# Performance work log

Measured on AMD Instinct MI355X. Metric: run time of the kernel, lower is better.

The kernel has to match this reference:

```python
import jax, jax.numpy as jnp
import numpy as np
from jax import lax

B, S, T = 16, 128, 64
V, E, H = 32000, 256, 256

def setup_inputs() -> dict:
    key = jax.random.key(0)
    ks = jax.random.split(key, 22)
    w = lambda k, shape: jax.random.normal(k, shape, dtype=jnp.float32) * 0.05
    return {
        "input_seq": jax.random.randint(ks[0], (B, S), 0, V),
        "target_seq": jax.random.randint(ks[1], (B, T), 0, V),
        "enc_emb": w(ks[2], (V, E)),
        "enc_Wih": w(ks[3], (4 * H, E)),
        "enc_Whh": w(ks[4], (4 * H, H)),
        "enc_b": w(ks[5], (4 * H,)),
        "dec_emb": w(ks[6], (V, E)),
        "Wq": w(ks[7], (H, H)), "bq": w(ks[8], (H,)),
        "Wk": w(ks[9], (H, H)), "bk": w(ks[10], (H,)),
        "Wv": w(ks[11], (H, H)), "bv": w(ks[12], (H,)),
        "Wo": w(ks[13], (H, H)), "bo": w(ks[14], (H,)),
        "dec_Wih": w(ks[15], (4 * H, E + H)),
        "dec_Whh": w(ks[16], (4 * H, H)),
        "dec_b": w(ks[17], (4 * H,)),
        "Wout": w(ks[18], (V, H)), "bout": w(ks[19], (V,)),
    }

def _lstm_step(Wih, Whh, b, x, h, c):
    # PyTorch LSTM gate order: i, f, g, o
    g = x @ Wih.T + h @ Whh.T + b
    i, f, gg, o = jnp.split(g, 4, axis=-1)
    c = jax.nn.sigmoid(f) * c + jax.nn.sigmoid(i) * jnp.tanh(gg)
    h = jax.nn.sigmoid(o) * jnp.tanh(c)
    return h, c

def reference(input_seq, target_seq, enc_emb, enc_Wih, enc_Whh, enc_b,
              dec_emb, Wq, bq, Wk, bk, Wv, bv, Wo, bo,
              dec_Wih, dec_Whh, dec_b, Wout, bout):
    Bn = input_seq.shape[0]
    # ---- encoder LSTM over source ----
    src = enc_emb[input_seq]                      # [B,S,E]
    h0 = jnp.zeros((Bn, H), src.dtype)
    c0 = jnp.zeros((Bn, H), src.dtype)

    def enc_step(carry, x_t):
        h, c = carry
        h, c = _lstm_step(enc_Wih, enc_Whh, enc_b, x_t, h, c)
        return (h, c), h
    (h_enc, c_enc), enc_hs = lax.scan(enc_step, (h0, c0), src.transpose(1, 0, 2))
    enc_out = enc_hs.transpose(1, 0, 2)           # [B,S,H]

    # ---- precompute attention K/V projections (enc_out is fixed) ----
    K = enc_out @ Wk.T + bk                       # [B,S,H]
    Vp = enc_out @ Wv.T + bv                      # [B,S,H]
    scale = 1.0 / jnp.sqrt(jnp.asarray(H, src.dtype))

    # ---- teacher-forced decode loop (sequential via scan) ----
    tok = dec_emb[target_seq[:, :-1]]             # [B,T-1,E]

    def dec_step(carry, x_t):
        h, c = carry
        q = h @ Wq.T + bq                         # [B,H]  query = current hidden
        scores = jnp.einsum('bh,bsh->bs', q, K) * scale
        attn = jax.nn.softmax(scores, axis=-1)
        ctx = jnp.einsum('bs,bsh->bh', attn, Vp)
        ctx = ctx @ Wo.T + bo                     # MHA out-projection
        h, c = _lstm_step(dec_Wih, dec_Whh, dec_b,
                          jnp.concatenate([x_t, ctx], axis=-1), h, c)
        logits = h @ Wout.T + bout                # [B,V]
        return (h, c), logits

    _, logits = lax.scan(dec_step, (h_enc, c_enc), tok.transpose(1, 0, 2))
    return logits.transpose(1, 0, 2)              # [B,T-1,V]
```

## Files before the change

### kernel.cpp

```cpp
#include <hip/hip_runtime.h>

typedef short bh8 __attribute__((ext_vector_type(8)));
typedef float f32x4 __attribute__((ext_vector_type(4)));

#define DEVI __device__ __forceinline__

union U8 { bh8 v; unsigned short u[8]; };

DEVI float bf2f(unsigned short u){
  unsigned int x = ((unsigned int)u) << 16;
  return __builtin_bit_cast(float, x);
}
DEVI unsigned short f2bf(float f){
  unsigned int u = __builtin_bit_cast(unsigned int, f);
  u += 0x7fffu + ((u >> 16) & 1u);
  return (unsigned short)(u >> 16);
}
DEVI float sigm(float x){ return 1.0f/(1.0f + __expf(-x)); }

DEVI f32x4 MFMA(bh8 a, bh8 b, f32x4 c){
  return __builtin_amdgcn_mfma_f32_16x16x32_bf16(a, b, c, 0, 0, 0);
}

DEVI unsigned int ld_sc0(const unsigned int* p){
  unsigned int v;
  asm volatile("global_load_dword %0, %1, off sc0\n\ts_waitcnt vmcnt(0)"
               : "=v"(v) : "v"(p) : "memory");
  return v;
}
DEVI void st_plain(unsigned int* p, unsigned int v){
  asm volatile("global_store_dword %0, %1, off" :: "v"(p), "v"(v) : "memory");
}

DEVI float poll2(const unsigned int* fastp, const unsigned int* slowp){
  unsigned int v;
  for (int it = 0; it < (1 << 23); ++it){
    v = ld_sc0(fastp);
    if (v != 0xFFFFFFFFu) return __builtin_bit_cast(float, v);
    v = __hip_atomic_load(slowp, __ATOMIC_RELAXED, __HIP_MEMORY_SCOPE_AGENT);
    if (v != 0xFFFFFFFFu) return __builtin_bit_cast(float, v);
  }
  return __builtin_bit_cast(float, v);
}

DEVI void conv_dev(const float* src, unsigned short* dst, int rows, int rstride,
                   int lblk, int nblk){
  int tid = threadIdx.x;
  size_t n = (size_t)rows * 128;
  for (size_t i = (size_t)lblk * 256 + tid; i < n; i += (size_t)nblk * 256){
    size_t r = i >> 7; int c = ((int)(i & 127)) * 2;
    const float* s = src + r * (size_t)rstride + c;
    unsigned int hp = (unsigned int)f2bf(s[0]) | ((unsigned int)f2bf(s[1]) << 16);
    *(unsigned int*)(dst + r * 256 + c) = hp;
  }
}

DEVI void fold_dev(const float* A, int offA, int sAm, int sAk,
                   const float* Bm, int offB, int sBn, int sBk,
                   const float* addM, float* Cf, unsigned short* Cb,
                   int M, int N, int lblk, int nblk){
  int tid = threadIdx.x;
  for (int i = lblk * 256 + tid; i < M * N; i += nblk * 256){
    int m = i / N, n = i - m * N;
    const float* a = A + offA + (size_t)m * sAm;
    const float* b = Bm + offB + (size_t)n * sBn;
    float acc = 0.f;
    for (int k = 0; k < 256; ++k) acc += a[(size_t)k * sAk] * b[(size_t)k * sBk];
    if (addM) acc += addM[m];
    if (Cf) Cf[i] = acc;
    if (Cb) Cb[i] = f2bf(acc);
  }
}

__global__ __launch_bounds__(256) void k_prepA(const int* input_seq, const int* target_seq,
      const float* enc_emb, const float* dec_emb,
      const float* enc_Wih, const float* dec_Wih, const float* Wout,
      const float* enc_Whh, const float* dec_Whh,
      const float* Wq, const float* Wk, const float* bq, const float* bk,
      const float* Wo, const float* bo, const float* dec_b,
      unsigned short* src_bf, unsigned short* tok_bf,
      unsigned short* wih_bf, unsigned short* wxd_bf, unsigned short* wout_bf,
      unsigned short* whhE_bf, unsigned short* whhD_bf,
      float* Gf, unsigned short* A3bf, float* c3f, float* c4f, float* c5f, float* xdb){
  int blk = blockIdx.x, tid = threadIdx.x;
  if (blk < 512){
    for (int r = 0; r < 4; ++r){
      int m = blk * 4 + r;
      int idx = input_seq[m];
      src_bf[(size_t)m * 256 + tid] = f2bf(enc_emb[(size_t)idx * 256 + tid]);
    }
  } else if (blk < 768){
    int lb = blk - 512;
    for (int r = 0; r < 4; ++r){
      int m = lb * 4 + r;
      if (m < 1008){
        int bb = m / 63, t = m - bb * 63;
        int idx = target_seq[bb * 64 + t];
        tok_bf[(size_t)m * 256 + tid] = f2bf(dec_emb[(size_t)idx * 256 + tid]);
      } else tok_bf[(size_t)m * 256 + tid] = 0;
    }
  }
  else if (blk < 896)  conv_dev(enc_Wih, wih_bf, 1024, 256, blk - 768, 128);
  else if (blk < 1024) conv_dev(dec_Wih, wxd_bf, 1024, 512, blk - 896, 128);
  else if (blk < 2048) conv_dev(Wout,    wout_bf, 32000, 256, blk - 1024, 1024);
  else if (blk < 2176) conv_dev(enc_Whh, whhE_bf, 1024, 256, blk - 2048, 128);
  else if (blk < 2304) conv_dev(dec_Whh, whhD_bf, 1024, 256, blk - 2176, 128);
  else if (blk < 3328) fold_dev(dec_Wih,256,512,1, Wo,0,1,256, nullptr, Gf,nullptr, 1024,256, blk - 2304, 1024);
  else if (blk < 3584) fold_dev(Wq,0,1,256,        Wk,0,1,256, nullptr, nullptr,A3bf, 256,256, blk - 3328, 256);
  else if (blk == 3584) fold_dev(bk,0,0,1, Wq,0,1,256, nullptr, c3f,nullptr, 1,256, 0, 1);
  else if (blk == 3585) fold_dev(bq,0,0,1, Wk,0,1,256, nullptr, c4f,nullptr, 1,256, 0, 1);
  else if (blk == 3586) fold_dev(bq,0,0,1, bk,0,0,1,   nullptr, c5f,nullptr, 1,1,   0, 1);
  else                  fold_dev(dec_Wih,256,512,1, bo,0,0,1, dec_b, xdb,nullptr, 1024,1, blk - 3587, 4);
}

__global__ __launch_bounds__(256) void k_prepB(const float* Gf, const float* Wv,
      const float* bv, unsigned short* A2bf, float* xdb){
  int blk = blockIdx.x;
  if (blk < 512) fold_dev(Gf,0,256,1, Wv,0,1,256, nullptr, nullptr,A2bf, 1024,256, blk, 512);
  else           fold_dev(Gf,0,256,1, bv,0,0,1,   xdb,     xdb,nullptr, 1024,1,   blk - 512, 4);
}

DEVI void gemm_tile(const unsigned short* __restrict__ A,
      const unsigned short* __restrict__ Bw, const float* __restrict__ bias,
      float* __restrict__ Cf, unsigned short* __restrict__ Cb, int Mlog, int N,
      int tmi, int tni, unsigned short* lA, unsigned short* lB){
  int tid = threadIdx.x;
  int lane = tid & 63, wave = tid >> 6;
  int wm = wave >> 1, wn = wave & 1;
  int kg = lane >> 4, l15 = lane & 15;
  size_t tm = tmi, tn = tni;
  f32x4 acc[4][4];
#pragma unroll
  for (int i = 0; i < 4; ++i)
#pragma unroll
    for (int j = 0; j < 4; ++j) acc[i][j] = (f32x4){0.f, 0.f, 0.f, 0.f};

  for (int ks = 0; ks < 8; ++ks){
    __syncthreads();
#pragma unroll
    for (int i = 0; i < 2; ++i){
      int slot = i * 256 + tid;
      int r = slot >> 2, sg = slot & 3;
      bh8 va = *reinterpret_cast<const bh8*>(A + (tm * 128 + r) * 256 + ks * 32 + sg * 8);
      *reinterpret_cast<bh8*>((char*)lA + r * 64 + ((sg ^ (r & 3)) << 4)) = va;
      bh8 vb = *reinterpret_cast<const bh8*>(Bw + (tn * 128 + r) * 256 + ks * 32 + sg * 8);
      *reinterpret_cast<bh8*>((char*)lB + r * 64 + ((sg ^ (r & 3)) << 4)) = vb;
    }
    __syncthreads();
    bh8 af[4], bfr[4];
#pragma unroll
    for (int mi = 0; mi < 4; ++mi){
      int r = wm * 64 + mi * 16 + l15;
      af[mi] = *reinterpret_cast<const bh8*>((char*)lA + r * 64 + ((kg ^ (r & 3)) << 4));
    }
#pragma unroll
    for (int ni = 0; ni < 4; ++ni){
      int r = wn * 64 + ni * 16 + l15;
      bfr[ni] = *reinterpret_cast<const bh8*>((char*)lB + r * 64 + ((kg ^ (r & 3)) << 4));
    }
#pragma unroll
    for (int mi = 0; mi < 4; ++mi)
#pragma unroll
      for (int ni = 0; ni < 4; ++ni)
        acc[mi][ni] = MFMA(af[mi], bfr[ni], acc[mi][ni]);
  }
#pragma unroll
  for (int ni = 0; ni < 4; ++ni){
    int col = (int)tn * 128 + wn * 64 + ni * 16 + l15;
    float bv = bias ? bias[col] : 0.f;
#pragma unroll
    for (int mi = 0; mi < 4; ++mi){
#pragma unroll
      for (int rg = 0; rg < 4; ++rg){
        int row = (int)tm * 128 + wm * 64 + mi * 16 + kg * 4 + rg;
        if (row < Mlog){
          float v = acc[mi][ni][rg] + bv;
          if (Cb) Cb[(size_t)row * N + col] = f2bf(v);
          else    Cf[(size_t)row * N + col] = v;
        }
      }
    }
  }
}

__global__ __launch_bounds__(256) void k_gemm(const unsigned short* __restrict__ A,
      const unsigned short* __restrict__ Bw, const float* __restrict__ bias,
      float* __restrict__ Cf, unsigned short* __restrict__ Cb, int Mlog, int N){
  __shared__ __align__(16) unsigned short lA[128 * 32];
  __shared__ __align__(16) unsigned short lB[128 * 32];
  gemm_tile(A, Bw, bias, Cf, Cb, Mlog, N, blockIdx.y, blockIdx.x, lA, lB);
}

__global__ __launch_bounds__(256) void k_gemmAB(const unsigned short* src_bf,
      const unsigned short* wih_bf, const float* enc_b, float* Xg,
      const unsigned short* tok_bf, const unsigned short* wxd_bf, const float* xdb, float* Xd){
  __shared__ __align__(16) unsigned short lA[128 * 32];
  __shared__ __align__(16) unsigned short lB[128 * 32];
  int blk = blockIdx.x;
  if (blk < 128) gemm_tile(src_bf, wih_bf, enc_b, Xg, nullptr, 2048, 1024, blk >> 3, blk & 7, lA, lB);
  else { int l = blk - 128; gemm_tile(tok_bf, wxd_bf, xdb, Xd, nullptr, 1024, 1024, l >> 3, l & 7, lA, lB); }
}

__global__ __launch_bounds__(256) void k_gemmPost(const unsigned short* enc_bf,
      const unsigned short* A3bf, const float* c3f, unsigned short* KWb,
      const unsigned short* A2bf, unsigned short* VWWT,
      const float* c4f, const float* c5f, float* sbf){
  __shared__ __align__(16) unsigned short lA[128 * 32];
  __shared__ __align__(16) unsigned short lB[128 * 32];
  int blk = blockIdx.x, tid = threadIdx.x;
  if (blk < 32) gemm_tile(enc_bf, A3bf, c3f, nullptr, KWb, 2048, 256, blk >> 1, blk & 1, lA, lB);
  else if (blk < 160){ int l = blk - 32; gemm_tile(A2bf, enc_bf, nullptr, nullptr, VWWT, 1024, 2048, l >> 4, l & 15, lA, lB); }
  else {
    int m = (blk - 160) * 256 + tid;
    const unsigned short* e = enc_bf + (size_t)m * 256;
    float a = 0.f;
    for (int k = 0; k < 256; ++k) a += bf2f(e[k]) * c4f[k];
    sbf[m] = a + c5f[0];
  }
}

__global__ __launch_bounds__(256) void k_enc_g(const unsigned short* __restrict__ Whh_bf,
      const float* __restrict__ Xg, unsigned short* __restrict__ enc_bf,
      float* hbEf, float* hbEs, float* hbDf, float* hbDs, float* cfin){
  __shared__ __align__(16) unsigned short Ws[128 * 256];
  __shared__ __align__(16) float h_l[256];
  __shared__ float part[256];
  int tid = threadIdx.x, blk = blockIdx.x;
  int b = blk & 15, sub = blk >> 4, j0 = sub * 32;
  int lr = tid >> 1, kh = tid & 1;

  for (int i = 0; i < 16; ++i){
    int id = i * 256 + tid;
    int slr = id >> 5, c = id & 31;
    int R = (slr >> 5) * 256 + j0 + (slr & 31);
    bh8 v = *reinterpret_cast<const bh8*>(Whh_bf + (size_t)R * 256 + c * 8);
    *reinterpret_cast<bh8*>((char*)Ws + slr * 512 + ((c ^ (slr & 31)) << 4)) = v;
  }
  h_l[tid] = 0.f;
  float creg = 0.f;
  int Rr = (lr >> 5) * 256 + j0 + (lr & 31);
  __syncthreads();

  for (int t = 0; t < 128; ++t){
    float xg = (kh == 0) ? Xg[(size_t)(b * 128 + t) * 1024 + Rr] : 0.f;
    if (t > 0 && (tid >> 5) != sub)
      h_l[tid] = poll2((const unsigned int*)hbEf + (size_t)t * 4096 + b * 256 + tid,
                       (const unsigned int*)hbEs + (size_t)t * 4096 + b * 256 + tid);
    __syncthreads();
    {
      float acc = xg;
#pragma unroll
      for (int ci = 0; ci < 16; ++ci){
        int chunk = kh * 16 + ci;
        U8 w; w.v = *reinterpret_cast<const bh8*>((char*)Ws + lr * 512 + ((chunk ^ (lr & 31)) << 4));
        float4 ha = *(const float4*)(h_l + chunk * 8);
        float4 hb = *(const float4*)(h_l + chunk * 8 + 4);
        acc += ha.x*bf2f(w.u[0]) + ha.y*bf2f(w.u[1]) + ha.z*bf2f(w.u[2]) + ha.w*bf2f(w.u[3]);
        acc += hb.x*bf2f(w.u[4]) + hb.y*bf2f(w.u[5]) + hb.z*bf2f(w.u[6]) + hb.w*bf2f(w.u[7]);
      }
      part[tid] = acc;
    }
    __syncthreads();
    if (tid < 32){
      float gi = part[tid*2]      + part[tid*2 + 1];
      float gf = part[(32+tid)*2] + part[(32+tid)*2 + 1];
      float gg = part[(64+tid)*2] + part[(64+tid)*2 + 1];
      float go = part[(96+tid)*2] + part[(96+tid)*2 + 1];
      float c = sigm(gf) * creg + sigm(gi) * tanhf(gg);
      float h = sigm(go) * tanhf(c);
      creg = c;
      int j = j0 + tid;
      h_l[j] = h;
      unsigned int hb = __builtin_bit_cast(unsigned int, h);
      if (t < 127){
        st_plain((unsigned int*)hbEf + (size_t)(t + 1) * 4096 + b * 256 + j, hb);
        __hip_atomic_store((unsigned int*)hbEs + (size_t)(t + 1) * 4096 + b * 256 + j, hb,
                           __ATOMIC_RELAXED, __HIP_MEMORY_SCOPE_AGENT);
      } else {
        hbDf[b * 256 + j] = h;
        hbDs[b * 256 + j] = h;
        cfin[b * 256 + j] = c;
      }
      enc_bf[(size_t)(b * 128 + t) * 256 + j] = f2bf(h);
    }
  }
}

__global__ __launch_bounds__(256) void k_dec_g(const unsigned short* __restrict__ Whh_bf,
      const float* __restrict__ Xd, const unsigned short* __restrict__ KW,
      const unsigned short* __restrict__ VWWT, const float* __restrict__ sb,
      float* hbDf, float* hbDs, const float* __restrict__ cfin,
      unsigned short* __restrict__ Hs){
  __shared__ __align__(16) unsigned short KW_l[128 * 256];
  __shared__ __align__(16) unsigned short Ws[128 * 256];
  __shared__ __align__(16) float h_l[256];
  __shared__ float part[256];
  __shared__ float sc_l[128];
  __shared__ float at_l[128];
  __shared__ float red0, red1;
  int tid = threadIdx.x, blk = blockIdx.x;
  int b = blk & 15, sub = blk >> 4, j0 = sub * 32;
  int ss = tid >> 1, kh = tid & 1;
  int lr = ss;

  for (int i = 0; i < 16; ++i){
    int id = i * 256 + tid;
    int row = id >> 5, c = id & 31;
    bh8 v = *reinterpret_cast<const bh8*>(KW + (size_t)(b * 128 + row) * 256 + c * 8);
    *reinterpret_cast<bh8*>((char*)KW_l + row * 512 + ((c ^ (row & 31)) << 4)) = v;
  }
  for (int i = 0; i < 16; ++i){
    int id = i * 256 + tid;
    int row = id >> 5, c = id & 31;
    int R = (row >> 5) * 256 + j0 + (row & 31);
    bh8 v = *reinterpret_cast<const bh8*>(Whh_bf + (size_t)R * 256 + c * 8);
    *reinterpret_cast<bh8*>((char*)Ws + row * 512 + ((c ^ (row & 31)) << 4)) = v;
  }
  int Rr = (lr >> 5) * 256 + j0 + (lr & 31);
  U8 vw[8];
#pragma unroll
  for (int ci = 0; ci < 8; ++ci)
    vw[ci].v = *reinterpret_cast<const bh8*>(VWWT + (size_t)Rr * 2048 + b * 128 + kh * 64 + ci * 8);
  float sbreg = (tid < 128) ? sb[b * 128 + tid] : 0.f;
  float creg = (tid < 32) ? cfin[b * 256 + j0 + tid] : 0.f;
  __syncthreads();

  for (int t = 0; t < 63; ++t){
    float xdreg = (kh == 0) ? Xd[(size_t)(b * 63 + t) * 1024 + Rr] : 0.f;
    if (t == 0 || (tid >> 5) != sub)
      h_l[tid] = poll2((const unsigned int*)hbDf + (size_t)t * 4096 + b * 256 + tid,
                       (const unsigned int*)hbDs + (size_t)t * 4096 + b * 256 + tid);
    __syncthreads();
    {
      float a = 0.f;
#pragma unroll
      for (int i = 0; i < 16; ++i){
        int ch = kh * 16 + i;
        U8 ku; ku.v = *reinterpret_cast<const bh8*>((char*)KW_l + ss * 512 + ((ch ^ (ss & 31)) << 4));
        const float* hp = h_l + ch * 8;
#pragma unroll
        for (int q = 0; q < 8; ++q) a += hp[q] * bf2f(ku.u[q]);
      }
      part[tid] = a;
    }
    __syncthreads();
    if (tid < 128) sc_l[tid] = (part[2 * tid] + part[2 * tid + 1] + sbreg) * 0.0625f;
    __syncthreads();
    if (tid < 64){
      float m = fmaxf(sc_l[tid], sc_l[tid + 64]);
      for (int o = 32; o; o >>= 1) m = fmaxf(m, __shfl_xor(m, o));
      if (tid == 0) red0 = m;
    }
    __syncthreads();
    if (tid < 128) sc_l[tid] = __expf(sc_l[tid] - red0);
    __syncthreads();
    if (tid < 64){
      float s = sc_l[tid] + sc_l[tid + 64];
      for (int o = 32; o; o >>= 1) s += __shfl_xor(s, o);
      if (tid == 0) red1 = s;
    }
    __syncthreads();
    if (tid < 128) at_l[tid] = sc_l[tid] / red1;
    __syncthreads();
    {
      float acc = xdreg;
#pragma unroll
      for (int ci = 0; ci < 16; ++ci){
        int ch = kh * 16 + ci;
        U8 w; w.v = *reinterpret_cast<const bh8*>((char*)Ws + lr * 512 + ((ch ^ (lr & 31)) << 4));
        float4 ha = *(const float4*)(h_l + ch * 8);
        float4 hb = *(const float4*)(h_l + ch * 8 + 4);
        acc += ha.x*bf2f(w.u[0]) + ha.y*bf2f(w.u[1]) + ha.z*bf2f(w.u[2]) + ha.w*bf2f(w.u[3]);
        acc += hb.x*bf2f(w.u[4]) + hb.y*bf2f(w.u[5]) + hb.z*bf2f(w.u[6]) + hb.w*bf2f(w.u[7]);
      }
#pragma unroll
      for (int ci = 0; ci < 8; ++ci){
        const float* ap = at_l + kh * 64 + ci * 8;
#pragma unroll
        for (int q = 0; q < 8; ++q) acc += ap[q] * bf2f(vw[ci].u[q]);
      }
      part[tid] = acc;
    }
    __syncthreads();
    if (tid < 32){
      float gi = part[tid*2]      + part[tid*2 + 1];
      float gf = part[(32+tid)*2] + part[(32+tid)*2 + 1];
      float gg = part[(64+tid)*2] + part[(64+tid)*2 + 1];
      float go = part[(96+tid)*2] + part[(96+tid)*2 + 1];
      float c = sigm(gf) * creg + sigm(gi) * tanhf(gg);
      float h = sigm(go) * tanhf(c);
      creg = c;
      int j = j0 + tid;
      h_l[j] = h;
      unsigned int hb = __builtin_bit_cast(unsigned int, h);
      st_plain((unsigned int*)hbDf + (size_t)(t + 1) * 4096 + b * 256 + j, hb);
      __hip_atomic_store((unsigned int*)hbDs + (size_t)(t + 1) * 4096 + b * 256 + j, hb,
                         __ATOMIC_RELAXED, __HIP_MEMORY_SCOPE_AGENT);
      Hs[(size_t)(b * 63 + t) * 256 + j] = f2bf(h);
    }
    __syncthreads();
  }
}

extern "C" void kernel_launch(void* const* d_in, const int* in_sizes, int n_in,
                              void* d_out, int out_size, void* d_ws, size_t ws_size,
                              hipStream_t stream){
  const int expect[20] = {2048, 1024, 8192000, 262144, 262144, 1024, 8192000,
                          65536, 256, 65536, 256, 65536, 256, 65536, 256,
                          524288, 262144, 1024, 8192000, 32000};
  if (n_in != 20 || out_size != 32256000) return;
  for (int i = 0; i < 20; ++i) if (in_sizes[i] != expect[i]) return;

  const int*   input_seq  = (const int*)  d_in[0];
  const int*   target_seq = (const int*)  d_in[1];
  const float* enc_emb    = (const float*)d_in[2];
  const float* enc_Wih    = (const float*)d_in[3];
  const float* enc_Whh    = (const float*)d_in[4];
  const float* enc_b      = (const float*)d_in[5];
  const float* dec_emb    = (const float*)d_in[6];
  const float* Wq         = (const float*)d_in[7];
  const float* bq         = (const float*)d_in[8];
  const float* Wk         = (const float*)d_in[9];
  const float* bk         = (const float*)d_in[10];
  const float* Wv         = (const float*)d_in[11];
  const float* bv         = (const float*)d_in[12];
  const float* Wo         = (const float*)d_in[13];
  const float* bo         = (const float*)d_in[14];
  const float* dec_Wih    = (const float*)d_in[15];
  const float* dec_Whh    = (const float*)d_in[16];
  const float* dec_b      = (const float*)d_in[17];
  const float* Wout       = (const float*)d_in[18];
  const float* bout       = (const float*)d_in[19];

  char* p = (char*)d_ws;
  auto alloc = [&](size_t sz)->char*{ char* r = p; p += (sz + 255) & ~(size_t)255; return r; };

  unsigned short* Hs     = (unsigned short*)alloc((size_t)1024 * 256 * 2);
  size_t zsz = (size_t)(p - (char*)d_ws);
  float*          hbEf   = (float*)         alloc((size_t)128 * 4096 * 4);
  float*          hbEs   = (float*)         alloc((size_t)128 * 4096 * 4);
  float*          hbDf   = (float*)         alloc((size_t)64 * 4096 * 4);
  float*          hbDs   = (float*)         alloc((size_t)64 * 4096 * 4);
  size_t ffend = (size_t)(p - (char*)d_ws);
  float*          cfin   = (float*)          alloc(16 * 256 * 4);
  unsigned short* src_bf  = (unsigned short*)alloc((size_t)2048 * 256 * 2);
  unsigned short* tok_bf  = (unsigned short*)alloc((size_t)1024 * 256 * 2);
  unsigned short* wih_bf  = (unsigned short*)alloc((size_t)1024 * 256 * 2);
  unsigned short* wxd_bf  = (unsigned short*)alloc((size_t)1024 * 256 * 2);
  unsigned short* wout_bf = (unsigned short*)alloc((size_t)32000 * 256 * 2);
  unsigned short* whhE_bf = (unsigned short*)alloc((size_t)1024 * 256 * 2);
  unsigned short* whhD_bf = (unsigned short*)alloc((size_t)1024 * 256 * 2);
  float*          Gf      = (float*)         alloc((size_t)1024 * 256 * 4);
  unsigned short* A3bf    = (unsigned short*)alloc((size_t)256 * 256 * 2);
  unsigned short* A2bf    = (unsigned short*)alloc((size_t)1024 * 256 * 2);
  float*          c3f     = (float*)         alloc(256 * 4);
  float*          c4f     = (float*)         alloc(256 * 4);
  float*          c5f     = (float*)         alloc(256);
  float*          xdb     = (float*)         alloc(1024 * 4);
  float*          Xg      = (float*)         alloc((size_t)2048 * 1024 * 4);
  float*          Xd      = (float*)         alloc((size_t)1024 * 1024 * 4);
  unsigned short* enc_bf  = (unsigned short*)alloc((size_t)2048 * 256 * 2);
  unsigned short* KWb     = (unsigned short*)alloc((size_t)2048 * 256 * 2);
  unsigned short* VWWT    = (unsigned short*)alloc((size_t)1024 * 2048 * 2);
  float*          sbf     = (float*)         alloc(2048 * 4);
  if ((size_t)(p - (char*)d_ws) > ws_size) return;

  hipMemsetAsync(d_ws, 0, zsz, stream);
  hipMemsetAsync((char*)d_ws + zsz, 0xFF, ffend - zsz, stream);
  hipMemsetAsync(hbEf, 0, 4096 * 4, stream);
  hipMemsetAsync(hbEs, 0, 4096 * 4, stream);

  k_prepA<<<3591, 256, 0, stream>>>(input_seq, target_seq, enc_emb, dec_emb,
      enc_Wih, dec_Wih, Wout, enc_Whh, dec_Whh, Wq, Wk, bq, bk, Wo, bo, dec_b,
      src_bf, tok_bf, wih_bf, wxd_bf, wout_bf, whhE_bf, whhD_bf,
      Gf, A3bf, c3f, c4f, c5f, xdb);
  k_prepB<<<516, 256, 0, stream>>>(Gf, Wv, bv, A2bf, xdb);

  k_gemmAB<<<192, 256, 0, stream>>>(src_bf, wih_bf, enc_b, Xg, tok_bf, wxd_bf, xdb, Xd);

  k_enc_g<<<128, 256, 0, stream>>>(whhE_bf, Xg, enc_bf, hbEf, hbEs, hbDf, hbDs, cfin);

  k_gemmPost<<<168, 256, 0, stream>>>(enc_bf, A3bf, c3f, KWb, A2bf, VWWT, c4f, c5f, sbf);

  k_dec_g<<<128, 256, 0, stream>>>(whhD_bf, Xd, KWb, VWWT, sbf, hbDf, hbDs, cfin, Hs);

  k_gemm<<<dim3(250, 8), 256, 0, stream>>>(Hs, wout_bf, bout, (float*)d_out, nullptr, 1008, 32000);
}
```

Baseline: 684.0 us.

## Fold workspace memsets into prep kernel and overlap decoder softmax with Whh matvec

Removes the four hipMemsetAsync calls and performs the zero/0xFF initialization of the Hs and hidden-state flag buffers inside extra blocks of k_prepA, which cuts launch overhead. In the decoder step kernel, softmax is collapsed into a single wave using register shuffles instead of several shared-memory passes with barriers. Meanwhile the other three waves compute the recurrent Whh matvec, so the softmax overlaps with most of that work and fewer __syncthreads are needed per timestep. The cost is a more complex thread-role mapping, and wave 0 still has to do its share of the matvec afterwards.

```diff
diff --git a/kernel.cpp b/kernel.cpp
--- a/kernel.cpp
+++ b/kernel.cpp
@@ -81,7 +81,8 @@
       unsigned short* src_bf, unsigned short* tok_bf,
       unsigned short* wih_bf, unsigned short* wxd_bf, unsigned short* wout_bf,
       unsigned short* whhE_bf, unsigned short* whhD_bf,
-      float* Gf, unsigned short* A3bf, float* c3f, float* c4f, float* c5f, float* xdb){
+      float* Gf, unsigned short* A3bf, float* c3f, float* c4f, float* c5f, float* xdb,
+      char* HsZ, char* ffB, char* h0a, char* h0b){
   int blk = blockIdx.x, tid = threadIdx.x;
   if (blk < 512){
     for (int r = 0; r < 4; ++r){
@@ -110,7 +111,21 @@
   else if (blk == 3584) fold_dev(bk,0,0,1, Wq,0,1,256, nullptr, c3f,nullptr, 1,256, 0, 1);
   else if (blk == 3585) fold_dev(bq,0,0,1, Wk,0,1,256, nullptr, c4f,nullptr, 1,256, 0, 1);
   else if (blk == 3586) fold_dev(bq,0,0,1, bk,0,0,1,   nullptr, c5f,nullptr, 1,1,   0, 1);
-  else                  fold_dev(dec_Wih,256,512,1, bo,0,0,1, dec_b, xdb,nullptr, 1024,1, blk - 3587, 4);
+  else if (blk < 3591)  fold_dev(dec_Wih,256,512,1, bo,0,0,1, dec_b, xdb,nullptr, 1024,1, blk - 3587, 4);
+  else if (blk < 3655){
+    int lb = blk - 3591;
+    uint4* d = (uint4*)(HsZ + (size_t)lb * 8192);
+    for (int i = 0; i < 2; ++i) d[i * 256 + tid] = (uint4){0u,0u,0u,0u};
+  } else {
+    int lb = blk - 3655;
+    char* base = ffB + (size_t)lb * 24576;
+    for (int i = 0; i < 6; ++i){
+      char* a = base + ((size_t)(i * 256 + tid)) * 16;
+      size_t o1 = (size_t)(a - h0a), o2 = (size_t)(a - h0b);
+      unsigned int v = (o1 < 16384 || o2 < 16384) ? 0u : 0xFFFFFFFFu;
+      *(uint4*)a = (uint4){v,v,v,v};
+    }
+  }
 }
 
 __global__ __launch_bounds__(256) void k_prepB(const float* Gf, const float* Wv,
@@ -295,13 +310,14 @@
   __shared__ __align__(16) unsigned short Ws[128 * 256];
   __shared__ __align__(16) float h_l[256];
   __shared__ float part[256];
-  __shared__ float sc_l[128];
+  __shared__ float part2[256];
   __shared__ float at_l[128];
-  __shared__ float red0, red1;
   int tid = threadIdx.x, blk = blockIdx.x;
   int b = blk & 15, sub = blk >> 4, j0 = sub * 32;
-  int ss = tid >> 1, kh = tid & 1;
-  int lr = ss;
+  int ss = tid >> 1, kh_s = tid & 1;
+  int w = (tid >= 64) ? (tid - 64) : (192 + tid);
+  int lrw = w >> 1, khw = w & 1;
+  int Rr = (lrw >> 5) * 256 + j0 + (lrw & 31);
 
   for (int i = 0; i < 16; ++i){
     int id = i * 256 + tid;
@@ -316,17 +332,16 @@
     bh8 v = *reinterpret_cast<const bh8*>(Whh_bf + (size_t)R * 256 + c * 8);
     *reinterpret_cast<bh8*>((char*)Ws + row * 512 + ((c ^ (row & 31)) << 4)) = v;
   }
-  int Rr = (lr >> 5) * 256 + j0 + (lr & 31);
   U8 vw[8];
 #pragma unroll
   for (int ci = 0; ci < 8; ++ci)
-    vw[ci].v = *reinterpret_cast<const bh8*>(VWWT + (size_t)Rr * 2048 + b * 128 + kh * 64 + ci * 8);
-  float sbreg = (tid < 128) ? sb[b * 128 + tid] : 0.f;
+    vw[ci].v = *reinterpret_cast<const bh8*>(VWWT + (size_t)Rr * 2048 + b * 128 + khw * 64 + ci * 8);
+  float sb0 = 0.f, sb1 = 0.f;
+  if (tid < 64){ sb0 = sb[b * 128 + tid]; sb1 = sb[b * 128 + tid + 64]; }
   float creg = (tid < 32) ? cfin[b * 256 + j0 + tid] : 0.f;
   __syncthreads();
 
   for (int t = 0; t < 63; ++t){
-    float xdreg = (kh == 0) ? Xd[(size_t)(b * 63 + t) * 1024 + Rr] : 0.f;
     if (t == 0 || (tid >> 5) != sub)
       h_l[tid] = poll2((const unsigned int*)hbDf + (size_t)t * 4096 + b * 256 + tid,
                        (const unsigned int*)hbDs + (size_t)t * 4096 + b * 256 + tid);
@@ -335,7 +350,7 @@
       float a = 0.f;
 #pragma unroll
       for (int i = 0; i < 16; ++i){
-        int ch = kh * 16 + i;
+        int ch = kh_s * 16 + i;
         U8 ku; ku.v = *reinterpret_cast<const bh8*>((char*)KW_l + ss * 512 + ((ch ^ (ss & 31)) << 4));
         const float* hp = h_l + ch * 8;
 #pragma unroll
@@ -344,49 +359,61 @@
       part[tid] = a;
     }
     __syncthreads();
-    if (tid < 128) sc_l[tid] = (part[2 * tid] + part[2 * tid + 1] + sbreg) * 0.0625f;
-    __syncthreads();
     if (tid < 64){
-      float m = fmaxf(sc_l[tid], sc_l[tid + 64]);
+      float s0 = (part[2 * tid]        + part[2 * tid + 1]        + sb0) * 0.0625f;
+      float s1 = (part[2 * (tid + 64)] + part[2 * (tid + 64) + 1] + sb1) * 0.0625f;
+      float m = fmaxf(s0, s1);
       for (int o = 32; o; o >>= 1) m = fmaxf(m, __shfl_xor(m, o));
-      if (tid == 0) red0 = m;
-    }
-    __syncthreads();
-    if (tid < 128) sc_l[tid] = __expf(sc_l[tid] - red0);
-    __syncthreads();
-    if (tid < 64){
-      float s = sc_l[tid] + sc_l[tid + 64];
-      for (int o = 32; o; o >>= 1) s += __shfl_xor(s, o);
-      if (tid == 0) red1 = s;
-    }
-    __syncthreads();
-    if (tid < 128) at_l[tid] = sc_l[tid] / red1;
-    __syncthreads();
-    {
-      float acc = xdreg;
+      float p0 = __expf(s0 - m), p1 = __expf(s1 - m);
+      float S = p0 + p1;
+      for (int o = 32; o; o >>= 1) S += __shfl_xor(S, o);
+      at_l[tid]      = p0 / S;
+      at_l[tid + 64] = p1 / S;
+    } else {
+      float xdv = (khw == 0) ? Xd[(size_t)(b * 63 + t) * 1024 + Rr] : 0.f;
+      float macc = 0.f;
 #pragma unroll
       for (int ci = 0; ci < 16; ++ci){
-        int ch = kh * 16 + ci;
-        U8 w; w.v = *reinterpret_cast<const bh8*>((char*)Ws + lr * 512 + ((ch ^ (lr & 31)) << 4));
+        int ch = khw * 16 + ci;
+        U8 ww; ww.v = *reinterpret_cast<const bh8*>((char*)Ws + lrw * 512 + ((ch ^ (lrw & 31)) << 4));
         float4 ha = *(const float4*)(h_l + ch * 8);
         float4 hb = *(const float4*)(h_l + ch * 8 + 4);
-        acc += ha.x*bf2f(w.u[0]) + ha.y*bf2f(w.u[1]) + ha.z*bf2f(w.u[2]) + ha.w*bf2f(w.u[3]);
-        acc += hb.x*bf2f(w.u[4]) + hb.y*bf2f(w.u[5]) + hb.z*bf2f(w.u[6]) + hb.w*bf2f(w.u[7]);
+        macc += ha.x*bf2f(ww.u[0]) + ha.y*bf2f(ww.u[1]) + ha.z*bf2f(ww.u[2]) + ha.w*bf2f(ww.u[3]);
+        macc += hb.x*bf2f(ww.u[4]) + hb.y*bf2f(ww.u[5]) + hb.z*bf2f(ww.u[6]) + hb.w*bf2f(ww.u[7]);
       }
+      part2[w] = macc + xdv;
+    }
+    __syncthreads();
+    {
+      float acc;
+      if (tid < 64){
+        float xdv = (khw == 0) ? Xd[(size_t)(b * 63 + t) * 1024 + Rr] : 0.f;
+        float macc = 0.f;
+#pragma unroll
+        for (int ci = 0; ci < 16; ++ci){
+          int ch = khw * 16 + ci;
+          U8 ww; ww.v = *reinterpret_cast<const bh8*>((char*)Ws + lrw * 512 + ((ch ^ (lrw & 31)) << 4));
+          float4 ha = *(const float4*)(h_l + ch * 8);
+          float4 hb = *(const float4*)(h_l + ch * 8 + 4);
+          macc += ha.x*bf2f(ww.u[0]) + ha.y*bf2f(ww.u[1]) + ha.z*bf2f(ww.u[2]) + ha.w*bf2f(ww.u[3]);
+          macc += hb.x*bf2f(ww.u[4]) + hb.y*bf2f(ww.u[5]) + hb.z*bf2f(ww.u[6]) + hb.w*bf2f(ww.u[7]);
+        }
+        acc = macc + xdv;
+      } else acc = part2[w];
 #pragma unroll
       for (int ci = 0; ci < 8; ++ci){
-        const float* ap = at_l + kh * 64 + ci * 8;
+        const float* ap = at_l + khw * 64 + ci * 8;
 #pragma unroll
         for (int q = 0; q < 8; ++q) acc += ap[q] * bf2f(vw[ci].u[q]);
       }
-      part[tid] = acc;
+      part2[w] = acc;
     }
     __syncthreads();
     if (tid < 32){
-      float gi = part[tid*2]      + part[tid*2 + 1];
-      float gf = part[(32+tid)*2] + part[(32+tid)*2 + 1];
-      float gg = part[(64+tid)*2] + part[(64+tid)*2 + 1];
-      float go = part[(96+tid)*2] + part[(96+tid)*2 + 1];
+      float gi = part2[tid*2]      + part2[tid*2 + 1];
+      float gf = part2[(32+tid)*2] + part2[(32+tid)*2 + 1];
+      float gg = part2[(64+tid)*2] + part2[(64+tid)*2 + 1];
+      float go = part2[(96+tid)*2] + part2[(96+tid)*2 + 1];
       float c = sigm(gf) * creg + sigm(gi) * tanhf(gg);
       float h = sigm(go) * tanhf(c);
       creg = c;
@@ -436,12 +463,10 @@
   auto alloc = [&](size_t sz)->char*{ char* r = p; p += (sz + 255) & ~(size_t)255; return r; };
 
   unsigned short* Hs     = (unsigned short*)alloc((size_t)1024 * 256 * 2);
-  size_t zsz = (size_t)(p - (char*)d_ws);
   float*          hbEf   = (float*)         alloc((size_t)128 * 4096 * 4);
   float*          hbEs   = (float*)         alloc((size_t)128 * 4096 * 4);
   float*          hbDf   = (float*)         alloc((size_t)64 * 4096 * 4);
   float*          hbDs   = (float*)         alloc((size_t)64 * 4096 * 4);
-  size_t ffend = (size_t)(p - (char*)d_ws);
   float*          cfin   = (float*)          alloc(16 * 256 * 4);
   unsigned short* src_bf  = (unsigned short*)alloc((size_t)2048 * 256 * 2);
   unsigned short* tok_bf  = (unsigned short*)alloc((size_t)1024 * 256 * 2);
@@ -465,15 +490,11 @@
   float*          sbf     = (float*)         alloc(2048 * 4);
   if ((size_t)(p - (char*)d_ws) > ws_size) return;
 
-  hipMemsetAsync(d_ws, 0, zsz, stream);
-  hipMemsetAsync((char*)d_ws + zsz, 0xFF, ffend - zsz, stream);
-  hipMemsetAsync(hbEf, 0, 4096 * 4, stream);
-  hipMemsetAsync(hbEs, 0, 4096 * 4, stream);
-
-  k_prepA<<<3591, 256, 0, stream>>>(input_seq, target_seq, enc_emb, dec_emb,
+  k_prepA<<<3911, 256, 0, stream>>>(input_seq, target_seq, enc_emb, dec_emb,
       enc_Wih, dec_Wih, Wout, enc_Whh, dec_Whh, Wq, Wk, bq, bk, Wo, bo, dec_b,
       src_bf, tok_bf, wih_bf, wxd_bf, wout_bf, whhE_bf, whhD_bf,
-      Gf, A3bf, c3f, c4f, c5f, xdb);
+      Gf, A3bf, c3f, c4f, c5f, xdb,
+      (char*)Hs, (char*)hbEf, (char*)hbEf, (char*)hbEs);
   k_prepB<<<516, 256, 0, stream>>>(Gf, Wv, bv, A2bf, xdb);
 
   k_gemmAB<<<192, 256, 0, stream>>>(src_bf, wih_bf, enc_b, Xg, tok_bf, wxd_bf, xdb, Xd);
```

After: 696.7 us. No clear change (+1.9%).
